# Performance work log

Measured on AMD Instinct MI355X. Metric: run time of the kernel, lower is better.

## Reference

```python
import jax, jax.numpy as jnp
import numpy as np

B, S, HID = 2, 2048, 2048
NH, HD = 16, 128
KVC, QC = 512, 1536


def _rope(x):
    # x: [B, H, S, D]; interleaved-pair rotation matching the torch view(..., D//2, 2)
    b, h, s, d = x.shape
    inv_freq = 1.0 / (10000.0 ** (jnp.arange(0, d, 2, dtype=jnp.float32) / d))  # [D/2]
    pos = jnp.arange(s, dtype=jnp.float32)
    sinusoid = pos[:, None] * inv_freq[None, :]  # [S, D/2]
    sin = jnp.sin(sinusoid)[None, None]  # [1,1,S,D/2]
    cos = jnp.cos(sinusoid)[None, None]
    xr = x.reshape(b, h, s, d // 2, 2)
    x1, x2 = xr[..., 0], xr[..., 1]
    out = jnp.stack([x1 * cos - x2 * sin, x1 * sin + x2 * cos], axis=-1)
    return out.reshape(b, h, s, d)


def setup_inputs() -> dict:
    key = jax.random.key(0)
    ks = jax.random.split(key, 14)
    def lin(k, fan_in, fan_out):
        lim = 1.0 / np.sqrt(fan_in)
        kw, kb = jax.random.split(k)
        W = jax.random.uniform(kw, (fan_in, fan_out), jnp.float32, -lim, lim)
        b = jax.random.uniform(kb, (fan_out,), jnp.float32, -lim, lim)
        return W, b
    x = jax.random.normal(ks[0], (B, S, HID), jnp.float32)
    # causal mask (positions with 0 are masked out)
    attention_mask = jnp.tril(jnp.ones((S, S), jnp.int32))[None, None]  # [1,1,S,S]
    W_dkv, b_dkv = lin(ks[1], HID, KVC)
    W_uk, b_uk = lin(ks[2], KVC, NH * HD)
    W_uv, b_uv = lin(ks[3], KVC, NH * HD)
    W_dq, b_dq = lin(ks[4], HID, QC)
    W_uq, b_uq = lin(ks[5], QC, NH * HD)
    W_o, b_o = lin(ks[6], NH * HD, HID)
    return dict(x=x, attention_mask=attention_mask,
                W_dkv=W_dkv, b_dkv=b_dkv, W_uk=W_uk, b_uk=b_uk,
                W_uv=W_uv, b_uv=b_uv, W_dq=W_dq, b_dq=b_dq,
                W_uq=W_uq, b_uq=b_uq, W_o=W_o, b_o=b_o)


def reference(x, attention_mask, W_dkv, b_dkv, W_uk, b_uk, W_uv, b_uv,
              W_dq, b_dq, W_uq, b_uq, W_o, b_o):
    b, s, _ = x.shape
    kv = x @ W_dkv + b_dkv                                   # [B,S,KVC]
    k = (kv @ W_uk + b_uk).reshape(b, s, NH, HD).transpose(0, 2, 1, 3)  # [B,H,S,D]
    v = (kv @ W_uv + b_uv).reshape(b, s, NH, HD).transpose(0, 2, 1, 3)
    q = ((x @ W_dq + b_dq) @ W_uq + b_uq).reshape(b, s, NH, HD).transpose(0, 2, 1, 3)
    q, k = _rope(q), _rope(k)
    scores = jnp.einsum('bhqd,bhkd->bhqk', q, k) / jnp.sqrt(jnp.float32(HD))
    scores = jnp.where(attention_mask == 0, jnp.float32(-1e9), scores)
    probs = jax.nn.softmax(scores, axis=-1)
    out = jnp.einsum('bhqk,bhkd->bhqd', probs, v)            # [B,H,S,D]
    out = out.transpose(0, 2, 1, 3).reshape(b, s, NH * HD)
    return out @ W_o + b_o
```

## Files before the change

kernel.cpp:

```cpp
#include <hip/hip_runtime.h>
#include <stdint.h>

typedef unsigned short u16;
typedef uint32_t u32;
typedef __attribute__((ext_vector_type(8))) short short8;
typedef __attribute__((ext_vector_type(4))) float f32x4;
typedef __attribute__((ext_vector_type(4))) u32 u32x4;
typedef __attribute__((ext_vector_type(2))) u32 u32x2;
typedef __attribute__((ext_vector_type(4))) unsigned short u16x4;

#define BS_ 4096
#define S_ 2048
#define HID_ 2048
#define KVB 64

__device__ __forceinline__ float bf2f(u16 u) { union { u32 i; float f; } v; v.i = ((u32)u) << 16; return v.f; }
__device__ __forceinline__ u16 f2bf(float f) {
  union { float f; u32 i; } v; v.f = f;
  u32 r = v.i + 0x7fffu + ((v.i >> 16) & 1u);
  return (u16)(r >> 16);
}

__device__ __forceinline__ void gload16(const void* gsrc, void* ldst) {
  __builtin_amdgcn_global_load_lds(
      (const __attribute__((address_space(1))) void*)gsrc,
      (__attribute__((address_space(3))) void*)ldst, 16, 0, 0);
}

__global__ __launch_bounds__(256) void conv_f2b(const float* __restrict__ in, u16* __restrict__ out, int n4) {
  int i = blockIdx.x * 256 + threadIdx.x;
  if (i < n4) {
    float4 v = ((const float4*)in)[i];
    u16x4 o;
    o.x = f2bf(v.x); o.y = f2bf(v.y); o.z = f2bf(v.z); o.w = f2bf(v.w);
    ((u16x4*)out)[i] = o;
  }
}

__global__ __launch_bounds__(256) void transpose_conv(const float* __restrict__ W, u16* __restrict__ WT,
                                                      int K, int N) {
  __shared__ float tile[64][65];
  const int t = threadIdx.x;
  const int kb = blockIdx.y * 64, nb = blockIdx.x * 64;
#pragma unroll
  for (int c = 0; c < 4; ++c) {
    int idx = c * 256 + t;
    int row = idx >> 4;
    int col4 = (idx & 15) * 4;
    float4 v = *(const float4*)&W[(size_t)(kb + row) * N + nb + col4];
    tile[row][col4 + 0] = v.x; tile[row][col4 + 1] = v.y;
    tile[row][col4 + 2] = v.z; tile[row][col4 + 3] = v.w;
  }
  __syncthreads();
#pragma unroll
  for (int c = 0; c < 4; ++c) {
    int idx = c * 256 + t;
    int n = idx >> 4;
    int k4 = (idx & 15) * 4;
    u16x4 o;
    o.x = f2bf(tile[k4 + 0][n]); o.y = f2bf(tile[k4 + 1][n]);
    o.z = f2bf(tile[k4 + 2][n]); o.w = f2bf(tile[k4 + 3][n]);
    *(u16x4*)&WT[(size_t)(nb + n) * K + kb + k4] = o;
  }
}

__global__ __launch_bounds__(256) void concat_bias(const float* __restrict__ b_dkv, const float* __restrict__ b_dq,
                                                   const float* __restrict__ b_uk, const float* __restrict__ b_uv,
                                                   float* __restrict__ bc1, float* __restrict__ bc2) {
  int i = blockIdx.x * 256 + threadIdx.x;
  if (i < 512) bc1[i] = b_dkv[i];
  else if (i < 2048) bc1[i] = b_dq[i - 512];
  else if (i < 4096) bc2[i - 2048] = b_uk[i - 2048];
  else if (i < 6144) bc2[i - 2048] = b_uv[i - 4096];
}

__global__ __launch_bounds__(256) void vtrans(const u16* __restrict__ KVin, u16* __restrict__ VT) {
  __shared__ u16 tile[64][136];
  const int t = threadIdx.x;
  const int st0 = blockIdx.x * 64;
  const int bh = blockIdx.y;
  const int bb = bh >> 4, h = bh & 15;
  const u16* src = KVin + (size_t)bb * S_ * 4096 + 2048 + (size_t)h * 128;
  u16* dst = VT + (size_t)bh * 128 * S_;
#pragma unroll
  for (int c = 0; c < 4; ++c) {
    int idx = c * 256 + t;
    int s = idx >> 4, ch = idx & 15;
    short8 v = *(const short8*)&src[(size_t)(st0 + s) * 4096 + ch * 8];
    *(short8*)&tile[s][ch * 8] = v;
  }
  __syncthreads();
#pragma unroll
  for (int c = 0; c < 4; ++c) {
    int idx = c * 256 + t;
    int d = idx >> 3, ch = idx & 7;
    short8 o;
#pragma unroll
    for (int j = 0; j < 8; ++j) o[j] = tile[ch * 8 + j][d];
    *(short8*)&dst[(size_t)d * S_ + st0 + ch * 8] = o;
  }
}

__global__ __launch_bounds__(256) void rope_table(float* __restrict__ cs) {
  int idx = blockIdx.x * 256 + threadIdx.x;
  int pos = idx >> 6, i = idx & 63;
  float inv = powf(10000.f, -(float)i / 64.f);
  float a = (float)pos * inv;
  cs[idx * 2] = cosf(a);
  cs[idx * 2 + 1] = sinf(a);
}

template <int OUTF32, int ROPE>
__global__ __launch_bounds__(256) void gemm_bt(const u16* __restrict__ A, int lda,
                                               const u16* __restrict__ BT,
                                               const float* __restrict__ bias,
                                               const float* __restrict__ cs,
                                               void* __restrict__ Cout,
                                               int M, int N, int K) {
  __shared__ u16 As[128 * 64];
  __shared__ u16 Bs[128 * 64];
  const int t = threadIdx.x;
  const int lane = t & 63, wave = t >> 6;
  const int wm = wave >> 1, wn = wave & 1;
  const int gx = gridDim.x;
  const int nwg = gx * gridDim.y;
  const int flat = blockIdx.y * gx + blockIdx.x;
  const int swz = (flat & 7) * (nwg >> 3) + (flat >> 3);
  const int tn = swz % gx, tm = swz / gx;
  const int r16 = lane & 15, q4 = lane >> 4;

  f32x4 acc[4][4];
#pragma unroll
  for (int m = 0; m < 4; ++m)
#pragma unroll
    for (int n = 0; n < 4; ++n) acc[m][n] = (f32x4){0.f, 0.f, 0.f, 0.f};

  for (int kt = 0; kt < K; kt += 64) {
#pragma unroll
    for (int c = 0; c < 4; ++c) {
      int idx = c * 256 + t;
      int row = idx >> 3, ch = idx & 7;
      gload16(&A[(size_t)(tm * 128 + row) * lda + kt + ch * 8], (char*)As + idx * 16);
      gload16(&BT[(size_t)(tn * 128 + row) * K + kt + ch * 8], (char*)Bs + idx * 16);
    }
    __syncthreads();
#pragma unroll
    for (int kk = 0; kk < 64; kk += 32) {
      short8 af[4], bfv[4];
#pragma unroll
      for (int m = 0; m < 4; ++m)
        af[m] = *(const short8*)&As[(wm * 64 + m * 16 + r16) * 64 + kk + q4 * 8];
#pragma unroll
      for (int n = 0; n < 4; ++n)
        bfv[n] = *(const short8*)&Bs[(wn * 64 + n * 16 + r16) * 64 + kk + q4 * 8];
      __builtin_amdgcn_s_setprio(1);
#pragma unroll
      for (int m = 0; m < 4; ++m)
#pragma unroll
        for (int n = 0; n < 4; ++n)
          acc[m][n] = __builtin_amdgcn_mfma_f32_16x16x32_bf16(bfv[n], af[m], acc[m][n], 0, 0, 0);
      __builtin_amdgcn_s_setprio(0);
    }
    __syncthreads();
  }
#pragma unroll
  for (int n = 0; n < 4; ++n) {
    int gc0 = tn * 128 + wn * 64 + n * 16 + q4 * 4;
    float4 bv4 = *(const float4*)&bias[gc0];
    const int i0 = (gc0 & 127) >> 1;
#pragma unroll
    for (int m = 0; m < 4; ++m) {
      int grow = tm * 128 + wm * 64 + m * 16 + r16;
      float v0 = acc[m][n][0] + bv4.x, v1 = acc[m][n][1] + bv4.y;
      float v2 = acc[m][n][2] + bv4.z, v3 = acc[m][n][3] + bv4.w;
      if (ROPE && gc0 < ROPE) {
        int s = grow & 2047;
        float4 cp = *(const float4*)&cs[((size_t)s * 64 + i0) * 2];
        float y0 = v0 * cp.x - v1 * cp.y;
        float y1 = v0 * cp.y + v1 * cp.x;
        float y2 = v2 * cp.z - v3 * cp.w;
        float y3 = v2 * cp.w + v3 * cp.z;
        v0 = y0; v1 = y1; v2 = y2; v3 = y3;
      }
      if (OUTF32) {
        float4 o; o.x = v0; o.y = v1; o.z = v2; o.w = v3;
        *(float4*)&((float*)Cout)[(size_t)grow * N + gc0] = o;
      } else {
        u16x4 o; o.x = f2bf(v0); o.y = f2bf(v1); o.z = f2bf(v2); o.w = f2bf(v3);
        *(u16x4*)&((u16*)Cout)[(size_t)grow * N + gc0] = o;
      }
    }
  }
}

__global__ __launch_bounds__(256, 1) void attn_kernel(const u16* __restrict__ Q, const u16* __restrict__ K,
                                                      int kld, const u16* __restrict__ VT,
                                                      u16* __restrict__ O) {
  __shared__ u16 Kl[2][KVB * 128];
  __shared__ u16 Vl[2][128 * KVB];
  __shared__ u16 Pl[4][40 * 64];
  const int t = threadIdx.x;
  const int lane = t & 63, w = t >> 6;
  const int r16 = lane & 15, q4 = lane >> 4;
  const int b = blockIdx.x;
  const int xcd = b & 7, r = b >> 3;
  const int p = r & 7, g = r >> 3;
  const int bh = xcd + 8 * g;
  const int bb = bh >> 4, h = bh & 15;
  const u16* Qb = Q + (size_t)bb * S_ * HID_ + (size_t)h * 128;
  const u16* Kb = K + (size_t)bb * S_ * kld + (size_t)h * 128;
  const u16* VTb = VT + (size_t)bh * 128 * S_;
  u16* Ob = O + (size_t)bb * S_ * HID_ + (size_t)h * 128;

  auto stage = [&](int buf, int kvbase) {
#pragma unroll
    for (int c = 0; c < 4; ++c) {
      int s = c * 256 + t;
      int row = s >> 4;
      int chs = (s & 15) ^ (row & 7);
      gload16(&Kb[(size_t)(kvbase + row) * kld + chs * 8], (char*)Kl[buf] + s * 16);
    }
#pragma unroll
    for (int c = 0; c < 4; ++c) {
      int s = c * 256 + t;
      int row = s >> 3;
      int chs = (s & 7) ^ (row & 7);
      gload16(&VTb[(size_t)row * S_ + kvbase + chs * 8], (char*)Vl[buf] + s * 16);
    }
  };

  u16* Pw = &Pl[w][0];
  const float SCALE = 0.08838834764831845f;

#pragma unroll
  for (int seg = 0; seg < 2; ++seg) {
    const int qt = seg ? (15 - p) : p;
    const int nt = 2 * qt + 2;
    const int qrow0 = qt * 128 + w * 32;

    short8 qf[2][4];
#pragma unroll
    for (int m = 0; m < 2; ++m)
#pragma unroll
      for (int dk = 0; dk < 4; ++dk)
        qf[m][dk] = *(const short8*)&Qb[(size_t)(qrow0 + m * 16 + r16) * HID_ + dk * 32 + q4 * 8];

    f32x4 ao[2][8];
    float mr[2], lr[2];
#pragma unroll
    for (int m = 0; m < 2; ++m) {
#pragma unroll
      for (int dn = 0; dn < 8; ++dn) ao[m][dn] = (f32x4){0.f, 0.f, 0.f, 0.f};
      mr[m] = -1e30f; lr[m] = 0.f;
    }

    stage(0, 0);
    __syncthreads();

    for (int ti = 0; ti < nt; ++ti) {
      const int buf = ti & 1;
      const int kv0 = ti * KVB;
      if (ti + 1 < nt) stage(buf ^ 1, kv0 + KVB);

      if (kv0 <= qrow0 + 31) {
        f32x4 sc[2][4];
#pragma unroll
        for (int m = 0; m < 2; ++m)
#pragma unroll
          for (int n = 0; n < 4; ++n) sc[m][n] = (f32x4){0.f, 0.f, 0.f, 0.f};
#pragma unroll
        for (int dk = 0; dk < 4; ++dk) {
          short8 kf[4];
#pragma unroll
          for (int n = 0; n < 4; ++n) {
            int kr = n * 16 + r16;
            int ba = (kr * 256 + dk * 64 + q4 * 16) ^ ((kr & 7) << 4);
            kf[n] = *(const short8*)((const char*)Kl[buf] + ba);
          }
          __builtin_amdgcn_s_setprio(1);
#pragma unroll
          for (int n = 0; n < 4; ++n)
#pragma unroll
            for (int m = 0; m < 2; ++m)
              sc[m][n] = __builtin_amdgcn_mfma_f32_16x16x32_bf16(kf[n], qf[m][dk], sc[m][n], 0, 0, 0);
          __builtin_amdgcn_s_setprio(0);
        }
        const bool nm = (kv0 + 63 > qrow0);
#pragma unroll
        for (int m = 0; m < 2; ++m) {
          const int q = qrow0 + m * 16 + r16;
#pragma unroll
          for (int n = 0; n < 4; ++n)
#pragma unroll
            for (int j = 0; j < 4; ++j) {
              float sv = sc[m][n][j] * SCALE;
              if (nm) {
                int kv = kv0 + n * 16 + q4 * 4 + j;
                if (kv > q) sv = -1e30f;
              }
              sc[m][n][j] = sv;
            }
        }
        float tm0[2];
#pragma unroll
        for (int m = 0; m < 2; ++m) {
          float tm = sc[m][0][0];
#pragma unroll
          for (int n = 0; n < 4; ++n)
#pragma unroll
            for (int j = 0; j < 4; ++j) tm = fmaxf(tm, sc[m][n][j]);
          tm = fmaxf(tm, __shfl_xor(tm, 16));
          tm = fmaxf(tm, __shfl_xor(tm, 32));
          tm0[m] = tm;
        }
        float growth = fmaxf(tm0[0] - mr[0], tm0[1] - mr[1]);
        if (!__all(growth <= 8.0f)) {
#pragma unroll
          for (int m = 0; m < 2; ++m) {
            float mnew = fmaxf(mr[m], tm0[m]);
            float fsc = __expf(mr[m] - mnew);
            lr[m] *= fsc; mr[m] = mnew;
#pragma unroll
            for (int dn = 0; dn < 8; ++dn) ao[m][dn] *= fsc;
          }
        }
#pragma unroll
        for (int m = 0; m < 2; ++m) {
          float ps = 0.f;
#pragma unroll
          for (int n = 0; n < 4; ++n)
#pragma unroll
            for (int j = 0; j < 4; ++j) {
              float pv = __expf(sc[m][n][j] - mr[m]);
              sc[m][n][j] = pv;
              ps += pv;
            }
          ps += __shfl_xor(ps, 16);
          ps += __shfl_xor(ps, 32);
          lr[m] += ps;
        }
#pragma unroll
        for (int m = 0; m < 2; ++m)
#pragma unroll
          for (int n = 0; n < 4; ++n) {
            u32 lo, hi;
            asm("v_cvt_pk_bf16_f32 %0, %1, %2" : "=v"(lo) : "v"(sc[m][n][0]), "v"(sc[m][n][1]));
            asm("v_cvt_pk_bf16_f32 %0, %1, %2" : "=v"(hi) : "v"(sc[m][n][2]), "v"(sc[m][n][3]));
            u32x2 pr; pr.x = lo; pr.y = hi;
            int ba = ((m * 16 + r16) * 128 + n * 32 + q4 * 8) ^ ((r16 & 7) << 4);
            *(u32x2*)((char*)Pw + ba) = pr;
          }
#pragma unroll
        for (int s = 0; s < 2; ++s) {
          short8 pb[2];
#pragma unroll
          for (int m = 0; m < 2; ++m) {
            int ba = ((m * 16 + r16) * 128 + s * 64 + q4 * 16) ^ ((r16 & 7) << 4);
            pb[m] = *(const short8*)((const char*)Pw + ba);
          }
          __builtin_amdgcn_s_setprio(1);
#pragma unroll
          for (int dn = 0; dn < 8; ++dn) {
            int dr = dn * 16 + r16;
            int bv = (dr * 128 + s * 64 + q4 * 16) ^ ((dr & 7) << 4);
            short8 vf = *(const short8*)((const char*)Vl[buf] + bv);
#pragma unroll
            for (int m = 0; m < 2; ++m)
              ao[m][dn] = __builtin_amdgcn_mfma_f32_16x16x32_bf16(vf, pb[m], ao[m][dn], 0, 0, 0);
          }
          __builtin_amdgcn_s_setprio(0);
        }
      }
      __syncthreads();
    }

#pragma unroll
    for (int m = 0; m < 2; ++m) {
      float inv = 1.f / lr[m];
      const int q = qrow0 + m * 16 + r16;
#pragma unroll
      for (int dn = 0; dn < 8; ++dn) {
        u16x4 o;
#pragma unroll
        for (int j = 0; j < 4; ++j) o[j] = f2bf(ao[m][dn][j] * inv);
        *(u16x4*)&Ob[(size_t)q * HID_ + dn * 16 + q4 * 4] = o;
      }
    }
    __syncthreads();
  }
}

extern "C" void kernel_launch(void* const* d_in, const int* in_sizes, int n_in,
                              void* d_out, int out_size, void* d_ws, size_t ws_size,
                              hipStream_t stream) {
  (void)in_sizes; (void)n_in; (void)out_size; (void)ws_size;
  const float* x     = (const float*)d_in[0];
  const float* W_dkv = (const float*)d_in[2];
  const float* b_dkv = (const float*)d_in[3];
  const float* W_uk  = (const float*)d_in[4];
  const float* b_uk  = (const float*)d_in[5];
  const float* W_uv  = (const float*)d_in[6];
  const float* b_uv  = (const float*)d_in[7];
  const float* W_dq  = (const float*)d_in[8];
  const float* b_dq  = (const float*)d_in[9];
  const float* W_uq  = (const float*)d_in[10];
  const float* b_uq  = (const float*)d_in[11];
  const float* W_o   = (const float*)d_in[12];
  const float* b_o   = (const float*)d_in[13];
  float* out = (float*)d_out;

  char* ws = (char*)d_ws;
  size_t off = 0;
  auto carve = [&](size_t bytes) { void* p = ws + off; off += (bytes + 255) & ~(size_t)255; return p; };
  u16* xb     = (u16*)carve((size_t)BS_ * 2048 * 2);
  u16* WdkvqT = (u16*)carve((size_t)2048 * 2048 * 2);
  u16* WukvT  = (u16*)carve((size_t)4096 * 512 * 2);
  u16* WuqT   = (u16*)carve((size_t)2048 * 1536 * 2);
  u16* WoT    = (u16*)carve((size_t)2048 * 2048 * 2);
  u16* kvq1   = (u16*)carve((size_t)BS_ * 2048 * 2);
  u16* kvbuf  = (u16*)carve((size_t)BS_ * 4096 * 2);
  u16* qb     = (u16*)carve((size_t)BS_ * 2048 * 2);
  u16* aob    = (u16*)carve((size_t)BS_ * 2048 * 2);
  float* cs   = (float*)carve((size_t)2048 * 64 * 2 * 4);
  float* bc1  = (float*)carve((size_t)2048 * 4);
  float* bc2  = (float*)carve((size_t)4096 * 4);
  u16* VT     = xb;

  conv_f2b<<<dim3(BS_ * 2048 / 4 / 256), 256, 0, stream>>>(x, xb, BS_ * 2048 / 4);
  transpose_conv<<<dim3(512 / 64, 2048 / 64), 256, 0, stream>>>(W_dkv, WdkvqT, 2048, 512);
  transpose_conv<<<dim3(1536 / 64, 2048 / 64), 256, 0, stream>>>(W_dq, WdkvqT + (size_t)512 * 2048, 2048, 1536);
  transpose_conv<<<dim3(2048 / 64, 512 / 64), 256, 0, stream>>>(W_uk, WukvT, 512, 2048);
  transpose_conv<<<dim3(2048 / 64, 512 / 64), 256, 0, stream>>>(W_uv, WukvT + (size_t)2048 * 512, 512, 2048);
  transpose_conv<<<dim3(2048 / 64, 1536 / 64), 256, 0, stream>>>(W_uq, WuqT, 1536, 2048);
  transpose_conv<<<dim3(2048 / 64, 2048 / 64), 256, 0, stream>>>(W_o, WoT, 2048, 2048);
  rope_table<<<dim3(512), 256, 0, stream>>>(cs);
  concat_bias<<<dim3(24), 256, 0, stream>>>(b_dkv, b_dq, b_uk, b_uv, bc1, bc2);

  gemm_bt<0, 0><<<dim3(2048 / 128, BS_ / 128), 256, 0, stream>>>(xb, 2048, WdkvqT, bc1, nullptr, kvq1, BS_, 2048, 2048);
  gemm_bt<0, 2048><<<dim3(4096 / 128, BS_ / 128), 256, 0, stream>>>(kvq1, 2048, WukvT, bc2, cs, kvbuf, BS_, 4096, 512);
  gemm_bt<0, 2048><<<dim3(2048 / 128, BS_ / 128), 256, 0, stream>>>(kvq1 + 512, 2048, WuqT, b_uq, cs, qb, BS_, 2048, 1536);

  vtrans<<<dim3(S_ / 64, 32), 256, 0, stream>>>(kvbuf, VT);

  attn_kernel<<<dim3(256), 256, 0, stream>>>(qb, kvbuf, 4096, VT, aob);

  gemm_bt<1, 0><<<dim3(2048 / 128, BS_ / 128), 256, 0, stream>>>(aob, 2048, WoT, b_o, nullptr, out, BS_, 2048, 2048);
}
```

Before: 317.4 us.

## Split attention KV range across wave pairs and merge partial softmax states

The attention kernel now processes 64-row query tiles with 512 blocks instead of 128-row tiles with 256 blocks. Within each block, two wave pairs handle alternate 32-key halves of each 64-key tile and merge their online-softmax states (max, sum, accumulator) through shared memory at the end. Launch bounds are raised to allow two blocks per CU. The aim is more parallelism and better load balance across CUs for causal attention. The cost is an extra shared-memory reduction, doubled Q and K/V staging relative to compute, and more barriers per tile.

Result: faster. 302.5 us (-4.7%).

```diff
diff --git a/kernel.cpp b/kernel.cpp
--- a/kernel.cpp
+++ b/kernel.cpp
@@ -12,7 +12,6 @@
 #define BS_ 4096
 #define S_ 2048
 #define HID_ 2048
-#define KVB 64
 
 __device__ __forceinline__ float bf2f(u16 u) { union { u32 i; float f; } v; v.i = ((u32)u) << 16; return v.f; }
 __device__ __forceinline__ u16 f2bf(float f) {
@@ -193,50 +192,60 @@
   }
 }
 
-__global__ __launch_bounds__(256, 1) void attn_kernel(const u16* __restrict__ Q, const u16* __restrict__ K,
+__global__ __launch_bounds__(256, 2) void attn_kernel(const u16* __restrict__ Q, const u16* __restrict__ K,
                                                       int kld, const u16* __restrict__ VT,
                                                       u16* __restrict__ O) {
-  __shared__ u16 Kl[2][KVB * 128];
-  __shared__ u16 Vl[2][128 * KVB];
-  __shared__ u16 Pl[4][40 * 64];
+  __shared__ char smem[75776];
+  u16* Kl = (u16*)smem;
+  u16* Vl = (u16*)(smem + 32768);
+  u16* Pl = (u16*)(smem + 65536);
+  float* ex = (float*)smem;
+
   const int t = threadIdx.x;
   const int lane = t & 63, w = t >> 6;
   const int r16 = lane & 15, q4 = lane >> 4;
+  const int par = w >> 1, sub = w & 1;
   const int b = blockIdx.x;
-  const int xcd = b & 7, r = b >> 3;
-  const int p = r & 7, g = r >> 3;
-  const int bh = xcd + 8 * g;
+  const int xcd = b & 7, u = b >> 3;
+  const int p = u & 15, g4 = u >> 4;
+  const int bh = g4 * 8 + xcd;
   const int bb = bh >> 4, h = bh & 15;
   const u16* Qb = Q + (size_t)bb * S_ * HID_ + (size_t)h * 128;
   const u16* Kb = K + (size_t)bb * S_ * kld + (size_t)h * 128;
   const u16* VTb = VT + (size_t)bh * 128 * S_;
   u16* Ob = O + (size_t)bb * S_ * HID_ + (size_t)h * 128;
 
-  auto stage = [&](int buf, int kvbase) {
-#pragma unroll
-    for (int c = 0; c < 4; ++c) {
-      int s = c * 256 + t;
-      int row = s >> 4;
-      int chs = (s & 15) ^ (row & 7);
-      gload16(&Kb[(size_t)(kvbase + row) * kld + chs * 8], (char*)Kl[buf] + s * 16);
-    }
-#pragma unroll
-    for (int c = 0; c < 4; ++c) {
-      int s = c * 256 + t;
-      int row = s >> 3;
-      int chs = (s & 7) ^ (row & 7);
-      gload16(&VTb[(size_t)row * S_ + kvbase + chs * 8], (char*)Vl[buf] + s * 16);
+  auto stage = [&](int rs, int kvbase) {
+#pragma unroll
+    for (int pp = 0; pp < 2; ++pp) {
+      int kvb = kvbase + pp * 32;
+      char* kd = (char*)(Kl + (size_t)(rs * 2 + pp) * 4096);
+      char* vd = (char*)(Vl + (size_t)(rs * 2 + pp) * 4096);
+#pragma unroll
+      for (int c = 0; c < 2; ++c) {
+        int s = c * 256 + t;
+        int row = s >> 4;
+        int ch = (s & 15) ^ (row & 7);
+        gload16(&Kb[(size_t)(kvb + row) * kld + ch * 8], kd + s * 16);
+      }
+#pragma unroll
+      for (int c = 0; c < 2; ++c) {
+        int s = c * 256 + t;
+        int row = s >> 2;
+        int ch = (s & 3) ^ ((row >> 1) & 3);
+        gload16(&VTb[(size_t)row * S_ + kvb + ch * 8], vd + s * 16);
+      }
     }
   };
 
-  u16* Pw = &Pl[w][0];
+  u16* Pw = Pl + (size_t)w * 1280;
   const float SCALE = 0.08838834764831845f;
 
 #pragma unroll
   for (int seg = 0; seg < 2; ++seg) {
-    const int qt = seg ? (15 - p) : p;
-    const int nt = 2 * qt + 2;
-    const int qrow0 = qt * 128 + w * 32;
+    const int qt = seg ? (31 - p) : p;
+    const int nr = qt + 1;
+    const int qrow0 = qt * 64 + sub * 32;
 
     short8 qf[2][4];
 #pragma unroll
@@ -257,40 +266,42 @@
     stage(0, 0);
     __syncthreads();
 
-    for (int ti = 0; ti < nt; ++ti) {
-      const int buf = ti & 1;
-      const int kv0 = ti * KVB;
-      if (ti + 1 < nt) stage(buf ^ 1, kv0 + KVB);
+    for (int r = 0; r < nr; ++r) {
+      const int rs = r & 1;
+      if (r + 1 < nr) stage(rs ^ 1, (r + 1) * 64);
+      const int kv0 = r * 64 + par * 32;
+      const u16* Kbuf = Kl + (size_t)(rs * 2 + par) * 4096;
+      const u16* Vbuf = Vl + (size_t)(rs * 2 + par) * 4096;
 
       if (kv0 <= qrow0 + 31) {
-        f32x4 sc[2][4];
+        f32x4 sc[2][2];
 #pragma unroll
         for (int m = 0; m < 2; ++m)
 #pragma unroll
-          for (int n = 0; n < 4; ++n) sc[m][n] = (f32x4){0.f, 0.f, 0.f, 0.f};
+          for (int n = 0; n < 2; ++n) sc[m][n] = (f32x4){0.f, 0.f, 0.f, 0.f};
 #pragma unroll
         for (int dk = 0; dk < 4; ++dk) {
-          short8 kf[4];
-#pragma unroll
-          for (int n = 0; n < 4; ++n) {
+          short8 kf[2];
+#pragma unroll
+          for (int n = 0; n < 2; ++n) {
             int kr = n * 16 + r16;
             int ba = (kr * 256 + dk * 64 + q4 * 16) ^ ((kr & 7) << 4);
-            kf[n] = *(const short8*)((const char*)Kl[buf] + ba);
+            kf[n] = *(const short8*)((const char*)Kbuf + ba);
           }
           __builtin_amdgcn_s_setprio(1);
 #pragma unroll
-          for (int n = 0; n < 4; ++n)
+          for (int n = 0; n < 2; ++n)
 #pragma unroll
             for (int m = 0; m < 2; ++m)
               sc[m][n] = __builtin_amdgcn_mfma_f32_16x16x32_bf16(kf[n], qf[m][dk], sc[m][n], 0, 0, 0);
           __builtin_amdgcn_s_setprio(0);
         }
-        const bool nm = (kv0 + 63 > qrow0);
+        const bool nm = (kv0 + 31 > qrow0);
 #pragma unroll
         for (int m = 0; m < 2; ++m) {
           const int q = qrow0 + m * 16 + r16;
 #pragma unroll
-          for (int n = 0; n < 4; ++n)
+          for (int n = 0; n < 2; ++n)
 #pragma unroll
             for (int j = 0; j < 4; ++j) {
               float sv = sc[m][n][j] * SCALE;
@@ -306,7 +317,7 @@
         for (int m = 0; m < 2; ++m) {
           float tm = sc[m][0][0];
 #pragma unroll
-          for (int n = 0; n < 4; ++n)
+          for (int n = 0; n < 2; ++n)
 #pragma unroll
             for (int j = 0; j < 4; ++j) tm = fmaxf(tm, sc[m][n][j]);
           tm = fmaxf(tm, __shfl_xor(tm, 16));
@@ -328,7 +339,7 @@
         for (int m = 0; m < 2; ++m) {
           float ps = 0.f;
 #pragma unroll
-          for (int n = 0; n < 4; ++n)
+          for (int n = 0; n < 2; ++n)
 #pragma unroll
             for (int j = 0; j < 4; ++j) {
               float pv = __expf(sc[m][n][j] - mr[m]);
@@ -342,51 +353,64 @@
 #pragma unroll
         for (int m = 0; m < 2; ++m)
 #pragma unroll
-          for (int n = 0; n < 4; ++n) {
+          for (int n = 0; n < 2; ++n) {
             u32 lo, hi;
             asm("v_cvt_pk_bf16_f32 %0, %1, %2" : "=v"(lo) : "v"(sc[m][n][0]), "v"(sc[m][n][1]));
             asm("v_cvt_pk_bf16_f32 %0, %1, %2" : "=v"(hi) : "v"(sc[m][n][2]), "v"(sc[m][n][3]));
             u32x2 pr; pr.x = lo; pr.y = hi;
-            int ba = ((m * 16 + r16) * 128 + n * 32 + q4 * 8) ^ ((r16 & 7) << 4);
+            int ba = (m * 16 + r16) * 80 + n * 32 + q4 * 8;
             *(u32x2*)((char*)Pw + ba) = pr;
           }
-#pragma unroll
-        for (int s = 0; s < 2; ++s) {
-          short8 pb[2];
-#pragma unroll
-          for (int m = 0; m < 2; ++m) {
-            int ba = ((m * 16 + r16) * 128 + s * 64 + q4 * 16) ^ ((r16 & 7) << 4);
-            pb[m] = *(const short8*)((const char*)Pw + ba);
+        short8 pb[2];
+#pragma unroll
+        for (int m = 0; m < 2; ++m)
+          pb[m] = *(const short8*)((const char*)Pw + (m * 16 + r16) * 80 + q4 * 16);
+        __builtin_amdgcn_s_setprio(1);
+#pragma unroll
+        for (int dn = 0; dn < 8; ++dn) {
+          int d = dn * 16 + r16;
+          int bv = d * 64 + ((q4 ^ ((d >> 1) & 3)) * 16);
+          short8 vf = *(const short8*)((const char*)Vbuf + bv);
+#pragma unroll
+          for (int m = 0; m < 2; ++m)
+            ao[m][dn] = __builtin_amdgcn_mfma_f32_16x16x32_bf16(vf, pb[m], ao[m][dn], 0, 0, 0);
+        }
+        __builtin_amdgcn_s_setprio(0);
+      }
+      __syncthreads();
+    }
+
+    {
+      float* exb = ex + (size_t)sub * 4352 + (size_t)lane * 68;
+      if (par == 1) {
+#pragma unroll
+        for (int m = 0; m < 2; ++m)
+#pragma unroll
+          for (int dn = 0; dn < 8; ++dn)
+            *(f32x4*)(exb + m * 32 + dn * 4) = ao[m][dn];
+        exb[64] = mr[0]; exb[65] = mr[1]; exb[66] = lr[0]; exb[67] = lr[1];
+      }
+      __syncthreads();
+      if (par == 0) {
+#pragma unroll
+        for (int m = 0; m < 2; ++m) {
+          float mB = exb[64 + m], lB = exb[66 + m];
+          float mx = fmaxf(mr[m], mB);
+          float wA = __expf(mr[m] - mx), wB = __expf(mB - mx);
+          float inv = 1.f / (lr[m] * wA + lB * wB);
+          const int q = qrow0 + m * 16 + r16;
+#pragma unroll
+          for (int dn = 0; dn < 8; ++dn) {
+            f32x4 ob = *(const f32x4*)(exb + m * 32 + dn * 4);
+            u16x4 o;
+#pragma unroll
+            for (int j = 0; j < 4; ++j) o[j] = f2bf((ao[m][dn][j] * wA + ob[j] * wB) * inv);
+            *(u16x4*)&Ob[(size_t)q * HID_ + dn * 16 + q4 * 4] = o;
           }
-          __builtin_amdgcn_s_setprio(1);
-#pragma unroll
-          for (int dn = 0; dn < 8; ++dn) {
-            int dr = dn * 16 + r16;
-            int bv = (dr * 128 + s * 64 + q4 * 16) ^ ((dr & 7) << 4);
-            short8 vf = *(const short8*)((const char*)Vl[buf] + bv);
-#pragma unroll
-            for (int m = 0; m < 2; ++m)
-              ao[m][dn] = __builtin_amdgcn_mfma_f32_16x16x32_bf16(vf, pb[m], ao[m][dn], 0, 0, 0);
-          }
-          __builtin_amdgcn_s_setprio(0);
         }
       }
       __syncthreads();
     }
-
-#pragma unroll
-    for (int m = 0; m < 2; ++m) {
-      float inv = 1.f / lr[m];
-      const int q = qrow0 + m * 16 + r16;
-#pragma unroll
-      for (int dn = 0; dn < 8; ++dn) {
-        u16x4 o;
-#pragma unroll
-        for (int j = 0; j < 4; ++j) o[j] = f2bf(ao[m][dn][j] * inv);
-        *(u16x4*)&Ob[(size_t)q * HID_ + dn * 16 + q4 * 4] = o;
-      }
-    }
-    __syncthreads();
   }
 }
 
@@ -442,7 +466,7 @@
 
   vtrans<<<dim3(S_ / 64, 32), 256, 0, stream>>>(kvbuf, VT);
 
-  attn_kernel<<<dim3(256), 256, 0, stream>>>(qb, kvbuf, 4096, VT, aob);
+  attn_kernel<<<dim3(512), 256, 0, stream>>>(qb, kvbuf, 4096, VT, aob);
 
   gemm_bt<1, 0><<<dim3(2048 / 128, BS_ / 128), 256, 0, stream>>>(aob, 2048, WoT, b_o, nullptr, out, BS_, 2048, 2048);
 }
```
